# Kernel optimization log

Measured on AMD Instinct MI355X. Metric: run time of the kernel, lower is better.

Reference implementation:

```python
import jax, jax.numpy as jnp
import numpy as np

KERNEL_NUM = 20

def _l2norm(x):
    # torch F.normalize: x / max(||x||, eps)
    n = jnp.sqrt(jnp.sum(x * x, axis=-1, keepdims=True))
    return x / jnp.maximum(n, 1e-12)

def setup_inputs() -> dict:
    key = jax.random.key(0)
    ks = jax.random.split(key, 5)
    B, C, H, S, E, V = 32, 5, 50, 20, 300, 60000
    return {
        "candidate_title": jax.random.randint(ks[0], (B, C, S), 0, V),
        "clicked_title": jax.random.randint(ks[1], (B, H, S), 0, V),
        "candidate_title_pad": jnp.ones((B, C, S), jnp.float32),
        "clicked_title_pad": jnp.ones((B, H, S), jnp.float32),
        "embedding": jax.random.normal(ks[2], (V, E), jnp.float32),
        "ltr_w": jax.random.normal(ks[3], (H * KERNEL_NUM, 1), jnp.float32) * 0.03,
        "ltr_b": jax.random.normal(ks[4], (1,), jnp.float32),
    }

def reference(candidate_title, clicked_title, candidate_title_pad, clicked_title_pad, embedding, ltr_w, ltr_b):
    B, C, S = candidate_title.shape
    H = clicked_title.shape[1]
    K = KERNEL_NUM
    dt = embedding.dtype
    mus = (-0.9 + 0.1 * jnp.arange(K, dtype=dt))                    # [K]
    sigmas = jnp.concatenate([jnp.full((K - 1,), 0.1, dt), jnp.full((1,), 0.001, dt)])
    cdd = _l2norm(embedding[candidate_title])                        # [B,C,S,E]
    his = _l2norm(embedding[clicked_title])                          # [B,H,S,E]
    sim = jnp.einsum('bcse,bhte->bchst', cdd, his)                   # [B,C,H,S,S]
    mask_his = clicked_title_pad[:, None, :, None, :, None]          # [B,1,H,1,S,1]
    mask_cdd = candidate_title_pad[:, :, None, :, None]              # [B,C,1,S,1]
    kern = jnp.exp(-((sim[..., None] - mus) ** 2) / (2.0 * sigmas ** 2)) * mask_his  # [B,C,H,S,S,K]
    pooling_sum = jnp.sum(kern, axis=4)                              # [B,C,H,S,K]
    log_pooling = jnp.log(jnp.clip(pooling_sum, 1e-10, None)) * mask_cdd * 0.01
    pooling_vectors = jnp.sum(log_pooling, axis=-2)                  # [B,C,H,K]
    score = pooling_vectors.reshape(B, C, H * K) @ ltr_w + ltr_b     # [B,C,1]
    score = jax.nn.log_softmax(score, axis=1)                        # cdd_size > 1 path
    return jnp.squeeze(score)                                        # [B,C]
```

## Files before the change

### kernel.cpp

```cpp
#include <hip/hip_runtime.h>
#include <hip/hip_fp16.h>

typedef _Float16 half8 __attribute__((ext_vector_type(8)));
typedef _Float16 half4v __attribute__((ext_vector_type(4)));
typedef float float4v __attribute__((ext_vector_type(4)));

#define E_DIM 300
#define KP 320
#define B_ 32
#define NROW_CDD 3200
#define NROW_HIS 32000
#define LDSTB 656

__global__ __launch_bounds__(256) void gather_norm(const int* __restrict__ cand,
                                                   const int* __restrict__ clk,
                                                   const float* __restrict__ emb,
                                                   _Float16* __restrict__ outH)
{
    int row  = blockIdx.x * 4 + (threadIdx.x >> 6);
    int lane = threadIdx.x & 63;
    int tok = (row < NROW_CDD) ? cand[row] : clk[row - NROW_CDD];
    const float* e = emb + (long)tok * E_DIM;
    float v[5];
    float ss = 0.f;
#pragma unroll
    for (int j = 0; j < 5; ++j) {
        int idx = lane + j * 64;
        float x = (idx < E_DIM) ? e[idx] : 0.f;
        v[j] = x;
        ss += x * x;
    }
#pragma unroll
    for (int off = 32; off; off >>= 1) ss += __shfl_xor(ss, off);
    float scale = 1.0f / fmaxf(sqrtf(ss), 1e-12f);
    _Float16* o = outH + (long)row * KP;
#pragma unroll
    for (int j = 0; j < 5; ++j) {
        int idx = lane + j * 64;
        o[idx] = (_Float16)((idx < E_DIM) ? v[j] * scale : 0.f);
    }
}

__global__ __launch_bounds__(512, 1) void sim_gemm(const _Float16* __restrict__ wsH,
                                                   _Float16* __restrict__ simW)
{
    __shared__ __align__(16) char Abuf[100 * LDSTB];
    __shared__ __align__(16) char Bbuf[125 * LDSTB];
    float* simT = (float*)Abuf;

    int b = blockIdx.y, ntile = blockIdx.x;
    int tid = threadIdx.x;
    int wave = tid >> 6, lane = tid & 63;
    int wm = wave >> 2, wn = wave & 3;
    int g = lane >> 4, r16 = lane & 15;

    const char* gA = (const char*)(wsH + (size_t)b * 100 * KP);
    const char* gB = (const char*)(wsH + (size_t)(NROW_CDD + b * 1000 + ntile * 125) * KP);

    for (int u = tid; u < 4000; u += 512) {
        int r = u / 40, c = u - r * 40;
        *(uint4*)(Abuf + ((r * LDSTB + c * 16) ^ ((r & 7) << 4))) = *(const uint4*)(gA + (size_t)u * 16);
    }
    for (int u = tid; u < 5000; u += 512) {
        int r = u / 40, c = u - r * 40;
        *(uint4*)(Bbuf + ((r * LDSTB + c * 16) ^ ((r & 7) << 4))) = *(const uint4*)(gB + (size_t)u * 16);
    }
    __syncthreads();

    float4v acc[4][2];
#pragma unroll
    for (int m = 0; m < 4; ++m)
#pragma unroll
        for (int n = 0; n < 2; ++n) acc[m][n] = (float4v){0.f, 0.f, 0.f, 0.f};

#pragma unroll 2
    for (int k = 0; k < 10; ++k) {
        half8 bf[2];
#pragma unroll
        for (int n = 0; n < 2; ++n) {
            int rB = wn * 32 + n * 16 + r16; if (rB > 124) rB = 124;
            bf[n] = *(const half8*)(Bbuf + ((rB * LDSTB + k * 64 + g * 16) ^ ((rB & 7) << 4)));
        }
#pragma unroll
        for (int m = 0; m < 4; ++m) {
            int rA = wm * 64 + m * 16 + r16; if (rA > 99) rA = 99;
            half8 af = *(const half8*)(Abuf + ((rA * LDSTB + k * 64 + g * 16) ^ ((rA & 7) << 4)));
#pragma unroll
            for (int n = 0; n < 2; ++n)
                acc[m][n] = __builtin_amdgcn_mfma_f32_16x16x32_f16(af, bf[n], acc[m][n], 0, 0, 0);
        }
    }
    __syncthreads();

#pragma unroll
    for (int m = 0; m < 4; ++m) {
        int rowb = wm * 64 + m * 16 + g * 4;
#pragma unroll
        for (int n = 0; n < 2; ++n) {
            int col = wn * 32 + n * 16 + r16;
            if (col < 125) {
#pragma unroll
                for (int j = 0; j < 4; ++j) {
                    int r = rowb + j;
                    if (r < 100) simT[r * 132 + col] = acc[m][n][j];
                }
            }
        }
    }
    __syncthreads();

    size_t obase = (size_t)b * 100000 + (size_t)ntile * 125;
    for (int u = tid; u < 12500; u += 512) {
        int r = u / 125, c = u - r * 125;
        simW[obase + (size_t)r * 1000 + c] = (_Float16)simT[r * 132 + c];
    }
}

__global__ __launch_bounds__(256) void knrm_pool(const _Float16* __restrict__ simW,
                                                 const float* __restrict__ cpad,
                                                 const float* __restrict__ hpad,
                                                 const float* __restrict__ ltr_w,
                                                 float* __restrict__ rowsum)
{
    __shared__ float sS[50 * 21];
    __shared__ float mS[50 * 21];
    __shared__ float wS[1000];
    __shared__ float part[4];

    int row = blockIdx.x;
    int b = row / 100;
    int tid = threadIdx.x;

    if (tid < 250) {
        int p = tid * 4;
        half4v hv = *(const half4v*)(simW + (size_t)row * 1000 + p);
        float4v mv = *(const float4v*)(hpad + (size_t)b * 1000 + p);
        *(float4v*)&wS[p] = *(const float4v*)(ltr_w + p);
#pragma unroll
        for (int q = 0; q < 4; ++q) {
            int pq = p + q, h = pq / 20, t = pq - h * 20;
            sS[h * 21 + t] = (float)hv[q];
            mS[h * 21 + t] = mv[q];
        }
    }
    __syncthreads();

    float val = 0.f;
    if (tid < 250) {
        int h = tid % 50, kq = tid / 50;
        float bj[4], cj[4];
        bool is19[4];
#pragma unroll
        for (int j = 0; j < 4; ++j) {
            float mu = -0.9f + 0.1f * (float)(kq * 4 + j);
            bj[j] = 100.0f * mu;
            cj[j] = -50.0f * mu * mu;
            is19[j] = (kq * 4 + j) == 19;
        }
        float psum0 = 0.f, psum1 = 0.f, psum2 = 0.f, psum3 = 0.f;
        const float* sp = sS + h * 21;
        const float* mp = mS + h * 21;
#pragma unroll 4
        for (int t = 0; t < 20; ++t) {
            float s  = sp[t];
            float mm = mp[t];
            float d  = s - 1.0f;
            float arg19 = -500000.0f * d * d;
            float a0 = is19[0] ? arg19 : fmaf(fmaf(-50.0f, s, bj[0]), s, cj[0]);
            float a1 = is19[1] ? arg19 : fmaf(fmaf(-50.0f, s, bj[1]), s, cj[1]);
            float a2 = is19[2] ? arg19 : fmaf(fmaf(-50.0f, s, bj[2]), s, cj[2]);
            float a3 = is19[3] ? arg19 : fmaf(fmaf(-50.0f, s, bj[3]), s, cj[3]);
            psum0 = fmaf(__expf(a0), mm, psum0);
            psum1 = fmaf(__expf(a1), mm, psum1);
            psum2 = fmaf(__expf(a2), mm, psum2);
            psum3 = fmaf(__expf(a3), mm, psum3);
        }
        const float* wp = wS + h * 20 + kq * 4;
        val  = __logf(fmaxf(psum0, 1e-10f)) * wp[0];
        val += __logf(fmaxf(psum1, 1e-10f)) * wp[1];
        val += __logf(fmaxf(psum2, 1e-10f)) * wp[2];
        val += __logf(fmaxf(psum3, 1e-10f)) * wp[3];
    }
#pragma unroll
    for (int off = 32; off; off >>= 1) val += __shfl_down(val, off);
    int wave = tid >> 6, lane = tid & 63;
    if (lane == 0) part[wave] = val;
    __syncthreads();
    if (tid == 0)
        rowsum[row] = (part[0] + part[1] + part[2] + part[3]) * 0.01f * cpad[row];
}

__global__ __launch_bounds__(64) void finalize(const float* __restrict__ rowsum,
                                               const float* __restrict__ ltr_b,
                                               float* __restrict__ out)
{
    int b = blockIdx.x;
    int tid = threadIdx.x;
    __shared__ float sc[5];
    if (tid < 5) {
        float a = ltr_b[0];
        const float* rp = rowsum + (b * 5 + tid) * 20;
#pragma unroll
        for (int s = 0; s < 20; ++s) a += rp[s];
        sc[tid] = a;
    }
    __syncthreads();
    if (tid < 5) {
        float m = fmaxf(fmaxf(fmaxf(sc[0], sc[1]), fmaxf(sc[2], sc[3])), sc[4]);
        float sum = 0.f;
#pragma unroll
        for (int i = 0; i < 5; ++i) sum += __expf(sc[i] - m);
        out[b * 5 + tid] = sc[tid] - m - __logf(sum);
    }
}

extern "C" void kernel_launch(void* const* d_in, const int* in_sizes, int n_in,
                              void* d_out, int out_size, void* d_ws, size_t ws_size,
                              hipStream_t stream)
{
    const int*   cand = (const int*)d_in[0];
    const int*   clk  = (const int*)d_in[1];
    const float* cpad = (const float*)d_in[2];
    const float* hpad = (const float*)d_in[3];
    const float* emb  = (const float*)d_in[4];
    const float* lw   = (const float*)d_in[5];
    const float* lb   = (const float*)d_in[6];
    float* out = (float*)d_out;

    _Float16* wsH  = (_Float16*)d_ws;
    _Float16* simW = (_Float16*)((char*)d_ws + (size_t)(NROW_CDD + NROW_HIS) * KP * 2);
    float* rowsum  = (float*)((char*)simW + (size_t)B_ * 100 * 1000 * 2);

    hipLaunchKernelGGL(gather_norm, dim3((NROW_CDD + NROW_HIS) / 4), dim3(256), 0, stream,
                       cand, clk, emb, wsH);
    hipLaunchKernelGGL(sim_gemm, dim3(8, B_), dim3(512), 0, stream, wsH, simW);
    hipLaunchKernelGGL(knrm_pool, dim3(NROW_CDD), dim3(256), 0, stream,
                       simW, cpad, hpad, lw, rowsum);
    hipLaunchKernelGGL(finalize, dim3(B_), dim3(64), 0, stream, rowsum, lb, out);
}
```

Before: 47.89 us.

## Fuse embedding gather into sim GEMM and apply L2 norms post-GEMM

Removes the separate gather_norm kernel. The GEMM blocks now gather embedding rows directly into LDS as unnormalized fp16 and accumulate each row's sum of squares. Inverse norms are stored in shared memory and applied to the similarity values during the output write. This drops the round trip of the fp16 workspace through global memory and one launch. In exchange, candidate rows are gathered redundantly by each of the 8 column tiles, LDS writes become scattered 2-byte stores, and unnormalized values are rounded to fp16 before scaling.

```diff
diff --git a/kernel.cpp b/kernel.cpp
--- a/kernel.cpp
+++ b/kernel.cpp
@@ -9,43 +9,17 @@
 #define KP 320
 #define B_ 32
 #define NROW_CDD 3200
-#define NROW_HIS 32000
 #define LDSTB 656
 
-__global__ __launch_bounds__(256) void gather_norm(const int* __restrict__ cand,
+__global__ __launch_bounds__(512, 1) void sim_gemm(const int* __restrict__ cand,
                                                    const int* __restrict__ clk,
                                                    const float* __restrict__ emb,
-                                                   _Float16* __restrict__ outH)
-{
-    int row  = blockIdx.x * 4 + (threadIdx.x >> 6);
-    int lane = threadIdx.x & 63;
-    int tok = (row < NROW_CDD) ? cand[row] : clk[row - NROW_CDD];
-    const float* e = emb + (long)tok * E_DIM;
-    float v[5];
-    float ss = 0.f;
-#pragma unroll
-    for (int j = 0; j < 5; ++j) {
-        int idx = lane + j * 64;
-        float x = (idx < E_DIM) ? e[idx] : 0.f;
-        v[j] = x;
-        ss += x * x;
-    }
-#pragma unroll
-    for (int off = 32; off; off >>= 1) ss += __shfl_xor(ss, off);
-    float scale = 1.0f / fmaxf(sqrtf(ss), 1e-12f);
-    _Float16* o = outH + (long)row * KP;
-#pragma unroll
-    for (int j = 0; j < 5; ++j) {
-        int idx = lane + j * 64;
-        o[idx] = (_Float16)((idx < E_DIM) ? v[j] * scale : 0.f);
-    }
-}
-
-__global__ __launch_bounds__(512, 1) void sim_gemm(const _Float16* __restrict__ wsH,
                                                    _Float16* __restrict__ simW)
 {
-    __shared__ __align__(16) char Abuf[100 * LDSTB];
-    __shared__ __align__(16) char Bbuf[125 * LDSTB];
+    __shared__ __align__(16) char Abuf[100 * LDSTB + 128];
+    __shared__ __align__(16) char Bbuf[125 * LDSTB + 128];
+    __shared__ float invA[100];
+    __shared__ float invB[125];
     float* simT = (float*)Abuf;
 
     int b = blockIdx.y, ntile = blockIdx.x;
@@ -54,16 +28,54 @@
     int wm = wave >> 2, wn = wave & 3;
     int g = lane >> 4, r16 = lane & 15;
 
-    const char* gA = (const char*)(wsH + (size_t)b * 100 * KP);
-    const char* gB = (const char*)(wsH + (size_t)(NROW_CDD + b * 1000 + ntile * 125) * KP);
-
-    for (int u = tid; u < 4000; u += 512) {
-        int r = u / 40, c = u - r * 40;
-        *(uint4*)(Abuf + ((r * LDSTB + c * 16) ^ ((r & 7) << 4))) = *(const uint4*)(gA + (size_t)u * 16);
-    }
-    for (int u = tid; u < 5000; u += 512) {
-        int r = u / 40, c = u - r * 40;
-        *(uint4*)(Bbuf + ((r * LDSTB + c * 16) ^ ((r & 7) << 4))) = *(const uint4*)(gB + (size_t)u * 16);
+    float ssA[13], ssB[16];
+#pragma unroll
+    for (int i = 0; i < 13; ++i) {
+        int r = wave + 8 * i;
+        ssA[i] = 0.f;
+        if (r < 100) {
+            int tok = cand[b * 100 + r];
+            const float* e = emb + (size_t)tok * E_DIM;
+#pragma unroll
+            for (int j = 0; j < 5; ++j) {
+                int idx = lane + 64 * j;
+                float x = (idx < E_DIM) ? e[idx] : 0.f;
+                ssA[i] += x * x;
+                *(_Float16*)(Abuf + ((r * LDSTB + idx * 2) ^ ((r & 7) << 4))) = (_Float16)x;
+            }
+        }
+    }
+#pragma unroll
+    for (int i = 0; i < 16; ++i) {
+        int r = wave + 8 * i;
+        ssB[i] = 0.f;
+        if (r < 125) {
+            int tok = clk[b * 1000 + ntile * 125 + r];
+            const float* e = emb + (size_t)tok * E_DIM;
+#pragma unroll
+            for (int j = 0; j < 5; ++j) {
+                int idx = lane + 64 * j;
+                float x = (idx < E_DIM) ? e[idx] : 0.f;
+                ssB[i] += x * x;
+                *(_Float16*)(Bbuf + ((r * LDSTB + idx * 2) ^ ((r & 7) << 4))) = (_Float16)x;
+            }
+        }
+    }
+#pragma unroll
+    for (int i = 0; i < 13; ++i) {
+        float ss = ssA[i];
+#pragma unroll
+        for (int o = 32; o; o >>= 1) ss += __shfl_xor(ss, o);
+        int r = wave + 8 * i;
+        if (r < 100 && lane == 0) invA[r] = 1.0f / fmaxf(sqrtf(ss), 1e-12f);
+    }
+#pragma unroll
+    for (int i = 0; i < 16; ++i) {
+        float ss = ssB[i];
+#pragma unroll
+        for (int o = 32; o; o >>= 1) ss += __shfl_xor(ss, o);
+        int r = wave + 8 * i;
+        if (r < 125 && lane == 0) invB[r] = 1.0f / fmaxf(sqrtf(ss), 1e-12f);
     }
     __syncthreads();
 
@@ -112,7 +124,8 @@
     size_t obase = (size_t)b * 100000 + (size_t)ntile * 125;
     for (int u = tid; u < 12500; u += 512) {
         int r = u / 125, c = u - r * 125;
-        simW[obase + (size_t)r * 1000 + c] = (_Float16)simT[r * 132 + c];
+        float v = simT[r * 132 + c] * invA[r] * invB[c];
+        simW[obase + (size_t)r * 1000 + c] = (_Float16)v;
     }
 }
 
@@ -227,13 +240,10 @@
     const float* lb   = (const float*)d_in[6];
     float* out = (float*)d_out;
 
-    _Float16* wsH  = (_Float16*)d_ws;
-    _Float16* simW = (_Float16*)((char*)d_ws + (size_t)(NROW_CDD + NROW_HIS) * KP * 2);
-    float* rowsum  = (float*)((char*)simW + (size_t)B_ * 100 * 1000 * 2);
-
-    hipLaunchKernelGGL(gather_norm, dim3((NROW_CDD + NROW_HIS) / 4), dim3(256), 0, stream,
-                       cand, clk, emb, wsH);
-    hipLaunchKernelGGL(sim_gemm, dim3(8, B_), dim3(512), 0, stream, wsH, simW);
+    _Float16* simW = (_Float16*)d_ws;
+    float* rowsum  = (float*)((char*)d_ws + (size_t)B_ * 100 * 1000 * 2);
+
+    hipLaunchKernelGGL(sim_gemm, dim3(8, B_), dim3(512), 0, stream, cand, clk, emb, simW);
     hipLaunchKernelGGL(knrm_pool, dim3(NROW_CDD), dim3(256), 0, stream,
                        simW, cpad, hpad, lw, rowsum);
     hipLaunchKernelGGL(finalize, dim3(B_), dim3(64), 0, stream, rowsum, lb, out);
```

Result: slower. 57.77 us (+20.6%).
